# Kernel tuning notes

Hardware: AMD Instinct MI355X
Metric: run time of the kernel (lower is better)

Reference implementation:

```python
import jax, jax.numpy as jnp
import numpy as np

NEG_INF = float('-inf')

def setup_inputs() -> dict:
    key = jax.random.key(0)
    k1, k2 = jax.random.split(key)
    B, T, S, H, D = 2, 2048, 2048, 8, 64
    q = jax.random.normal(k1, (B, T, H, D), dtype=jnp.float32)
    kv = jax.random.normal(k2, (B, S, 2, H, D), dtype=jnp.float32)
    key_padding_mask = jnp.ones((B, S), dtype=bool)  # True = valid key
    return {"q": q, "kv": kv, "key_padding_mask": key_padding_mask, "causal": 1}


def reference(q, kv, key_padding_mask, causal):
    # q: (B,T,H,D), kv: (B,S,2,H,D)
    k = kv[:, :, 0]  # (B,S,H,D)
    v = kv[:, :, 1]  # (B,S,H,D)
    D = q.shape[-1]
    scale = D ** (-0.5)
    # scores: (B,H,T,S)
    scores = jnp.einsum('bthd,bshd->bhts', q, k) * scale
    # mask: True means "mask out" (matches torch masked_fill semantics)
    mask = ~key_padding_mask[:, None, None, :]  # (B,1,1,S)
    if causal:
        T, S = scores.shape[2], scores.shape[3]
        causal_mask = jnp.triu(jnp.ones((T, S), dtype=bool), k=1)  # (T,S)
        mask = mask | causal_mask[None, None, :, :]
    scores = jnp.where(mask, NEG_INF, scores)
    attn = jax.nn.softmax(scores, axis=-1)
    out = jnp.einsum('bhts,bshd->bthd', attn, v)  # (B,T,H,D)
    return out
```

## Files before the change

### kernel.cpp

```cpp
#include <hip/hip_runtime.h>
#include <hip/hip_bf16.h>

typedef __bf16 bf8_t __attribute__((ext_vector_type(8)));
typedef float  f4_t  __attribute__((ext_vector_type(4)));
typedef int    i4_t  __attribute__((ext_vector_type(4)));

constexpr int Bc = 2;
constexpr int Tc = 2048;
constexpr int Sc = 2048;
constexpr int Hc = 8;
constexpr int Dc = 64;
constexpr int BQ = 64;
constexpr int BK = 32;
constexpr int nQB = Tc / BQ;
constexpr int NKT = Sc / BK;
constexpr int NP  = nQB / 2;
constexpr int NS  = 4;
constexpr int TILE_H = 4096;
constexpr int KH = 2048;
constexpr int KTH = 4096;

__device__ __forceinline__ void g2l16(const void* g, void* l) {
    __builtin_amdgcn_global_load_lds(
        (const __attribute__((address_space(1))) void*)g,
        (__attribute__((address_space(3))) void*)l, 16, 0, 0);
}

__device__ __forceinline__ int pack_bf16(float lo, float hi) {
    const unsigned l16 = (unsigned)__builtin_bit_cast(unsigned short, (__bf16)lo);
    const unsigned h16 = (unsigned)__builtin_bit_cast(unsigned short, (__bf16)hi);
    return (int)(l16 | (h16 << 16));
}

__global__ __launch_bounds__(256)
void fa_prep(const float* __restrict__ kv, const int* __restrict__ kpm,
             __bf16* __restrict__ kvb, unsigned* __restrict__ kpmw)
{
    const int idx    = blockIdx.x * 256 + threadIdx.x;
    const int tile   = idx >> 9;
    const int within = idx & 511;
    const int b  = tile >> 9;
    const int h  = (tile >> 6) & 7;
    const int s0 = (tile & 63) * BK;
    __bf16* dst = kvb + (size_t)tile * TILE_H + within * 8;
    bf8_t o;
    if (within < 256) {
        const int row = within >> 3;
        const int col = ((within & 7) * 8) ^ ((row & 7) << 3);
        const float* src = kv + (((size_t)(b * Sc + s0 + row) * 2 + 0) * Hc + h) * Dc + col;
        const float4 x0 = *(const float4*)src;
        const float4 x1 = *(const float4*)(src + 4);
        o[0] = (__bf16)x0.x; o[1] = (__bf16)x0.y; o[2] = (__bf16)x0.z; o[3] = (__bf16)x0.w;
        o[4] = (__bf16)x1.x; o[5] = (__bf16)x1.y; o[6] = (__bf16)x1.z; o[7] = (__bf16)x1.w;
    } else {
        const int c    = within - 256;
        const int vrow = c >> 2;
        const int sc   = (c & 3) * 8;
        const float* src = kv + (((size_t)(b * Sc + s0 + sc) * 2 + 1) * Hc + h) * Dc + vrow;
        #pragma unroll
        for (int j = 0; j < 8; ++j) o[j] = (__bf16)src[(size_t)j * 2 * Hc * Dc];
    }
    *(bf8_t*)dst = o;

    if (idx < Bc * NKT) {
        const int bb = idx >> 6, tt = idx & 63;
        unsigned m = 0;
        for (int k = 0; k < 32; ++k)
            m |= (kpm[bb * Sc + tt * BK + k] != 0 ? 1u : 0u) << k;
        kpmw[idx] = m;
    }
}

__global__ __launch_bounds__(256, 4)
void fa_part(const float* __restrict__ q,
             const __bf16* __restrict__ kvb,
             const unsigned* __restrict__ kpmw,
             const int* __restrict__ causal_p,
             float* __restrict__ part_o,
             float* __restrict__ part_l)
{
    __shared__ __bf16 shK[3 * KTH];

    const int tid  = threadIdx.x;
    const int wave = tid >> 6;
    const int lane = tid & 63;
    const int n16  = lane & 15;
    const int quad = lane >> 4;

    const int bid = blockIdx.x;
    const int h   = bid & 7;
    const int g   = bid >> 3;
    const int b   = g / (NP * NS);
    const int rem = g % (NP * NS);
    const int p   = rem / NS;
    const int s   = rem % NS;
    const int causal = causal_p[0];

    const int nA   = causal ? (nQB - p)  : 32;
    const int nB   = causal ? (p + 1)    : 32;
    const int ntot = nA + nB;
    const int lo   = (ntot * s + NS - 1) / NS;
    const int hi   = (ntot * (s + 1) + NS - 1) / NS;

    const __bf16* kvt = kvb + (size_t)((b * Hc + h) * NKT) * TILE_H;
    const unsigned* mw_b = kpmw + b * NKT;

    const int kA_off = n16 * 64 + ((quad * 8) ^ ((n16 & 7) << 3));
    const int lds_st = tid * 8;
    const int vOff   = n16 * 32 + quad * 8;
    const int addrA  = (n16 + ((quad & 1) << 5)) << 2;
    const int addrB  = addrA + 64;
    const bool hiQ   = quad >= 2;
    const float scale = 0.125f;

    #pragma unroll 1
    for (int seg = 0; seg < 2; ++seg) {
        const int qt = seg ? p : (nQB - 1 - p);
        const int t0 = seg ? (max(lo, nA) - nA) : lo;
        const int t1 = seg ? (hi - nA)          : min(hi, nA);
        if (t0 >= t1) continue;

        __syncthreads();

        const int q_base = qt * BQ;
        const int tqn    = q_base + wave * 16 + n16;

        bf8_t a_q[2];
        {
            const float* qrow = q + ((size_t)(b * Tc + tqn) * Hc + h) * Dc;
            #pragma unroll
            for (int f = 0; f < 2; ++f) {
                const float4 x0 = *(const float4*)(qrow + f * 32 + quad * 8);
                const float4 x1 = *(const float4*)(qrow + f * 32 + quad * 8 + 4);
                bf8_t v;
                v[0] = (__bf16)(x0.x * scale); v[1] = (__bf16)(x0.y * scale);
                v[2] = (__bf16)(x0.z * scale); v[3] = (__bf16)(x0.w * scale);
                v[4] = (__bf16)(x1.x * scale); v[5] = (__bf16)(x1.y * scale);
                v[6] = (__bf16)(x1.z * scale); v[7] = (__bf16)(x1.w * scale);
                a_q[f] = v;
            }
        }

        f4_t o_acc[4];
        #pragma unroll
        for (int dt = 0; dt < 4; ++dt) o_acc[dt] = (f4_t){0.f, 0.f, 0.f, 0.f};
        float lsum = 0.f;

        int cu = 0, nx = KTH, nn = 2 * KTH;
        {
            const __bf16* src = kvt + (size_t)(2 * t0) * TILE_H;
            g2l16(src + lds_st,          &shK[lds_st]);
            g2l16(src + TILE_H + lds_st, &shK[2048 + lds_st]);
        }

        for (int it = t0; it < t1; ++it) {
            const int kb = it * 64;
            const unsigned cm0 = mw_b[2 * it];
            const unsigned cm1 = mw_b[2 * it + 1];

            const __bf16* vb0 = kvt + (size_t)(2 * it) * TILE_H + KH + vOff;
            const __bf16* vb1 = vb0 + TILE_H;
            const bf8_t bv0 = *(const bf8_t*)(vb0);
            const bf8_t bv1 = *(const bf8_t*)(vb0 + 512);
            const bf8_t bv2 = *(const bf8_t*)(vb0 + 1024);
            const bf8_t bv3 = *(const bf8_t*)(vb0 + 1536);

            if (it + 1 < t1) {
                const __bf16* srcn = kvt + (size_t)(2 * (it + 1)) * TILE_H;
                g2l16(srcn + lds_st,          &shK[nx + lds_st]);
                g2l16(srcn + TILE_H + lds_st, &shK[nx + 2048 + lds_st]);
                asm volatile("s_waitcnt vmcnt(6)" ::: "memory");
            } else {
                asm volatile("s_waitcnt vmcnt(4)" ::: "memory");
            }
            __builtin_amdgcn_s_barrier();

            const bf8_t bv4 = *(const bf8_t*)(vb1);
            const bf8_t bv5 = *(const bf8_t*)(vb1 + 512);
            const bf8_t bv6 = *(const bf8_t*)(vb1 + 1024);
            const bf8_t bv7 = *(const bf8_t*)(vb1 + 1536);

            #pragma unroll
            for (int hh = 0; hh < 2; ++hh) {
                const unsigned cmw = hh ? cm1 : cm0;
                int pk[2][2];
                #pragma unroll
                for (int sub = 0; sub < 2; ++sub) {
                    const int kbase = cu + hh * 2048 + sub * 1024;
                    const bf8_t bk0 = *(const bf8_t*)&shK[kbase + kA_off];
                    const bf8_t bk1 = *(const bf8_t*)&shK[kbase + (kA_off ^ 32)];
                    f4_t acc = (f4_t){0.f, 0.f, 0.f, 0.f};
                    __builtin_amdgcn_s_setprio(1);
                    acc = __builtin_amdgcn_mfma_f32_16x16x32_bf16(bk0, a_q[0], acc, 0, 0, 0);
                    acc = __builtin_amdgcn_mfma_f32_16x16x32_bf16(bk1, a_q[1], acc, 0, 0, 0);
                    __builtin_amdgcn_s_setprio(0);
                    const int keyb = kb + hh * 32 + sub * 16 + quad * 4;
                    const unsigned mb = cmw >> (sub * 16 + quad * 4);
                    float pv[4];
                    #pragma unroll
                    for (int r = 0; r < 4; ++r) {
                        const bool valid = ((mb >> r) & 1u) && (!causal || keyb + r <= tqn);
                        const float pp = valid ? __expf(acc[r] - 8.0f) : 0.0f;
                        lsum += pp;
                        pv[r] = pp;
                    }
                    pk[sub][0] = pack_bf16(pv[0], pv[1]);
                    pk[sub][1] = pack_bf16(pv[2], pv[3]);
                }

                const int a0 = __builtin_amdgcn_ds_bpermute(addrA, pk[0][0]);
                const int a1 = __builtin_amdgcn_ds_bpermute(addrA, pk[0][1]);
                const int b0 = __builtin_amdgcn_ds_bpermute(addrB, pk[0][0]);
                const int b1 = __builtin_amdgcn_ds_bpermute(addrB, pk[0][1]);
                const int c0 = __builtin_amdgcn_ds_bpermute(addrA, pk[1][0]);
                const int c1 = __builtin_amdgcn_ds_bpermute(addrA, pk[1][1]);
                const int d0 = __builtin_amdgcn_ds_bpermute(addrB, pk[1][0]);
                const int d1 = __builtin_amdgcn_ds_bpermute(addrB, pk[1][1]);
                union { i4_t i; bf8_t b; } u;
                u.i[0] = hiQ ? c0 : a0;
                u.i[1] = hiQ ? c1 : a1;
                u.i[2] = hiQ ? d0 : b0;
                u.i[3] = hiQ ? d1 : b1;
                const bf8_t a_p = u.b;

                __builtin_amdgcn_s_setprio(1);
                if (hh == 0) {
                    o_acc[0] = __builtin_amdgcn_mfma_f32_16x16x32_bf16(a_p, bv0, o_acc[0], 0, 0, 0);
                    o_acc[1] = __builtin_amdgcn_mfma_f32_16x16x32_bf16(a_p, bv1, o_acc[1], 0, 0, 0);
                    o_acc[2] = __builtin_amdgcn_mfma_f32_16x16x32_bf16(a_p, bv2, o_acc[2], 0, 0, 0);
                    o_acc[3] = __builtin_amdgcn_mfma_f32_16x16x32_bf16(a_p, bv3, o_acc[3], 0, 0, 0);
                } else {
                    o_acc[0] = __builtin_amdgcn_mfma_f32_16x16x32_bf16(a_p, bv4, o_acc[0], 0, 0, 0);
                    o_acc[1] = __builtin_amdgcn_mfma_f32_16x16x32_bf16(a_p, bv5, o_acc[1], 0, 0, 0);
                    o_acc[2] = __builtin_amdgcn_mfma_f32_16x16x32_bf16(a_p, bv6, o_acc[2], 0, 0, 0);
                    o_acc[3] = __builtin_amdgcn_mfma_f32_16x16x32_bf16(a_p, bv7, o_acc[3], 0, 0, 0);
                }
                __builtin_amdgcn_s_setprio(0);
            }

            const int tswap = cu; cu = nx; nx = nn; nn = tswap;
        }

        lsum += __shfl_xor(lsum, 16);
        lsum += __shfl_xor(lsum, 32);
        float l_row[4];
        #pragma unroll
        for (int r = 0; r < 4; ++r) {
            const int li = __builtin_amdgcn_ds_bpermute((quad * 4 + r) << 2,
                                                        __builtin_bit_cast(int, lsum));
            l_row[r] = __builtin_bit_cast(float, li);
        }

        const size_t slot = (size_t)(((b * Hc + h) * NP + p) * NS + s) * 2 + seg;
        float* po = part_o + slot * (BQ * Dc);
        #pragma unroll
        for (int dt = 0; dt < 4; ++dt) {
            #pragma unroll
            for (int r = 0; r < 4; ++r) {
                const int row = wave * 16 + quad * 4 + r;
                po[row * Dc + dt * 16 + n16] = o_acc[dt][r];
            }
        }
        if (n16 == 0) {
            #pragma unroll
            for (int r = 0; r < 4; ++r) {
                const int row = wave * 16 + quad * 4 + r;
                part_l[slot * BQ + row] = l_row[r];
            }
        }
    }
}

__global__ __launch_bounds__(256, 4)
void fa_reduce(const float* __restrict__ part_o,
               const float* __restrict__ part_l,
               const int* __restrict__ causal_p,
               float* __restrict__ out)
{
    const int gtid = blockIdx.x * 256 + threadIdx.x;
    const int e    = gtid & (BQ * Dc / 4 - 1);
    const int qi   = gtid >> 10;
    const int row  = e >> 4;
    const int d4   = e & 15;

    const int qt = qi & (nQB - 1);
    const int h  = (qi >> 5) & (Hc - 1);
    const int b  = qi >> 8;
    const int causal = causal_p[0];

    const int p    = (qt < NP) ? qt : (nQB - 1 - qt);
    const int seg  = (qt < NP) ? 1 : 0;
    const int nA   = causal ? (nQB - p) : 32;
    const int nB   = causal ? (p + 1)   : 32;
    const int ntot = nA + nB;
    const int segLo = seg ? nA : 0;
    const int segHi = seg ? ntot : nA;

    float4 acc = make_float4(0.f, 0.f, 0.f, 0.f);
    float  l   = 0.f;
    #pragma unroll
    for (int s = 0; s < NS; ++s) {
        const int lo = (ntot * s + NS - 1) / NS;
        const int hi = (ntot * (s + 1) + NS - 1) / NS;
        if (lo < segHi && segLo < hi && lo < hi) {
            const size_t slot = (size_t)(((b * Hc + h) * NP + p) * NS + s) * 2 + seg;
            const float4 v = *(const float4*)(part_o + slot * (BQ * Dc) + row * Dc + d4 * 4);
            acc.x += v.x; acc.y += v.y; acc.z += v.z; acc.w += v.w;
            l += part_l[slot * BQ + row];
        }
    }
    const float inv = 1.0f / l;
    const int t = qt * BQ + row;
    float4 o;
    o.x = acc.x * inv; o.y = acc.y * inv; o.z = acc.z * inv; o.w = acc.w * inv;
    *(float4*)(out + ((size_t)(b * Tc + t) * Hc + h) * Dc + d4 * 4) = o;
}

extern "C" void kernel_launch(void* const* d_in, const int* in_sizes, int n_in,
                              void* d_out, int out_size, void* d_ws, size_t ws_size,
                              hipStream_t stream) {
    const float* q   = (const float*)d_in[0];
    const float* kv  = (const float*)d_in[1];
    const int*   kpm = (const int*)d_in[2];
    const int*   cz  = (const int*)d_in[3];
    float*       out = (float*)d_out;

    __bf16* kvb = (__bf16*)d_ws;
    const size_t kvb_bytes = (size_t)Bc * Hc * NKT * TILE_H * sizeof(__bf16);
    unsigned* kpmw = (unsigned*)((char*)d_ws + kvb_bytes);
    float* part_o  = (float*)((char*)d_ws + kvb_bytes + 4096);

    const size_t nslots = (size_t)Bc * Hc * NP * NS * 2;
    float* part_l = part_o + nslots * (BQ * Dc);

    const int grid0 = Bc * Hc * NKT * 512 / 256;
    fa_prep<<<grid0, 256, 0, stream>>>(kv, kpm, kvb, kpmw);

    const int grid1 = Bc * Hc * NP * NS;
    fa_part<<<grid1, 256, 0, stream>>>(q, kvb, kpmw, cz, part_o, part_l);

    const int grid2 = (int)((size_t)Bc * Hc * nQB * (BQ * Dc / 4) / 256);
    fa_reduce<<<grid2, 256, 0, stream>>>(part_o, part_l, cz, out);
}
```

Measured before the change: 114.1 us.

## Stage V tiles through LDS with swizzled layout and double buffering

V tiles were previously loaded straight from global memory into registers each iteration. Now they are staged into LDS alongside K using async global-to-LDS copies, with the prep kernel writing V in a swizzled layout to avoid bank conflicts. The triple-buffered K ring becomes a double-buffered K+V slot, which adds a second barrier per iteration. The aim is to take the global-load latency for V off the critical path, at the cost of more LDS traffic and extra synchronisation.

```diff
diff --git a/kernel.cpp b/kernel.cpp
--- a/kernel.cpp
+++ b/kernel.cpp
@@ -18,7 +18,7 @@
 constexpr int NS  = 4;
 constexpr int TILE_H = 4096;
 constexpr int KH = 2048;
-constexpr int KTH = 4096;
+constexpr int SLOT_H = 8192;
 
 __device__ __forceinline__ void g2l16(const void* g, void* l) {
     __builtin_amdgcn_global_load_lds(
@@ -42,8 +42,8 @@
     const int b  = tile >> 9;
     const int h  = (tile >> 6) & 7;
     const int s0 = (tile & 63) * BK;
-    __bf16* dst = kvb + (size_t)tile * TILE_H + within * 8;
     bf8_t o;
+    __bf16* dst;
     if (within < 256) {
         const int row = within >> 3;
         const int col = ((within & 7) * 8) ^ ((row & 7) << 3);
@@ -52,13 +52,17 @@
         const float4 x1 = *(const float4*)(src + 4);
         o[0] = (__bf16)x0.x; o[1] = (__bf16)x0.y; o[2] = (__bf16)x0.z; o[3] = (__bf16)x0.w;
         o[4] = (__bf16)x1.x; o[5] = (__bf16)x1.y; o[6] = (__bf16)x1.z; o[7] = (__bf16)x1.w;
+        dst = kvb + (size_t)tile * TILE_H + within * 8;
     } else {
         const int c    = within - 256;
         const int vrow = c >> 2;
-        const int sc   = (c & 3) * 8;
-        const float* src = kv + (((size_t)(b * Sc + s0 + sc) * 2 + 1) * Hc + h) * Dc + vrow;
+        const int g8   = c & 3;
+        const float* src = kv + (((size_t)(b * Sc + s0 + g8 * 8) * 2 + 1) * Hc + h) * Dc + vrow;
         #pragma unroll
         for (int j = 0; j < 8; ++j) o[j] = (__bf16)src[(size_t)j * 2 * Hc * Dc];
+        const int r  = vrow >> 1;
+        const int gg = ((vrow & 1) * 4 + g8) ^ (r & 7);
+        dst = kvb + (size_t)tile * TILE_H + KH + r * 64 + gg * 8;
     }
     *(bf8_t*)dst = o;
 
@@ -79,7 +83,7 @@
              float* __restrict__ part_o,
              float* __restrict__ part_l)
 {
-    __shared__ __bf16 shK[3 * KTH];
+    __shared__ __bf16 shKV[2 * SLOT_H];
 
     const int tid  = threadIdx.x;
     const int wave = tid >> 6;
@@ -106,8 +110,9 @@
     const unsigned* mw_b = kpmw + b * NKT;
 
     const int kA_off = n16 * 64 + ((quad * 8) ^ ((n16 & 7) << 3));
+    const int vRd    = (n16 >> 1) * 64 +
+                       ((((n16 & 1) << 2) | quad) ^ (n16 >> 1)) * 8;
     const int lds_st = tid * 8;
-    const int vOff   = n16 * 32 + quad * 8;
     const int addrA  = (n16 + ((quad & 1) << 5)) << 2;
     const int addrB  = addrA + 64;
     const bool hiQ   = quad >= 2;
@@ -146,39 +151,32 @@
         for (int dt = 0; dt < 4; ++dt) o_acc[dt] = (f4_t){0.f, 0.f, 0.f, 0.f};
         float lsum = 0.f;
 
-        int cu = 0, nx = KTH, nn = 2 * KTH;
+        int cu = 0;
         {
             const __bf16* src = kvt + (size_t)(2 * t0) * TILE_H;
-            g2l16(src + lds_st,          &shK[lds_st]);
-            g2l16(src + TILE_H + lds_st, &shK[2048 + lds_st]);
+            g2l16(src + lds_st,               &shKV[lds_st]);
+            g2l16(src + TILE_H + lds_st,      &shKV[2048 + lds_st]);
+            g2l16(src + KH + lds_st,          &shKV[4096 + lds_st]);
+            g2l16(src + TILE_H + KH + lds_st, &shKV[6144 + lds_st]);
         }
 
         for (int it = t0; it < t1; ++it) {
             const int kb = it * 64;
             const unsigned cm0 = mw_b[2 * it];
             const unsigned cm1 = mw_b[2 * it + 1];
-
-            const __bf16* vb0 = kvt + (size_t)(2 * it) * TILE_H + KH + vOff;
-            const __bf16* vb1 = vb0 + TILE_H;
-            const bf8_t bv0 = *(const bf8_t*)(vb0);
-            const bf8_t bv1 = *(const bf8_t*)(vb0 + 512);
-            const bf8_t bv2 = *(const bf8_t*)(vb0 + 1024);
-            const bf8_t bv3 = *(const bf8_t*)(vb0 + 1536);
+            const int nx = cu ^ SLOT_H;
 
             if (it + 1 < t1) {
                 const __bf16* srcn = kvt + (size_t)(2 * (it + 1)) * TILE_H;
-                g2l16(srcn + lds_st,          &shK[nx + lds_st]);
-                g2l16(srcn + TILE_H + lds_st, &shK[nx + 2048 + lds_st]);
-                asm volatile("s_waitcnt vmcnt(6)" ::: "memory");
+                g2l16(srcn + lds_st,               &shKV[nx + lds_st]);
+                g2l16(srcn + TILE_H + lds_st,      &shKV[nx + 2048 + lds_st]);
+                g2l16(srcn + KH + lds_st,          &shKV[nx + 4096 + lds_st]);
+                g2l16(srcn + TILE_H + KH + lds_st, &shKV[nx + 6144 + lds_st]);
+                asm volatile("s_waitcnt vmcnt(4)" ::: "memory");
             } else {
-                asm volatile("s_waitcnt vmcnt(4)" ::: "memory");
+                asm volatile("s_waitcnt vmcnt(0)" ::: "memory");
             }
             __builtin_amdgcn_s_barrier();
-
-            const bf8_t bv4 = *(const bf8_t*)(vb1);
-            const bf8_t bv5 = *(const bf8_t*)(vb1 + 512);
-            const bf8_t bv6 = *(const bf8_t*)(vb1 + 1024);
-            const bf8_t bv7 = *(const bf8_t*)(vb1 + 1536);
 
             #pragma unroll
             for (int hh = 0; hh < 2; ++hh) {
@@ -187,8 +185,8 @@
                 #pragma unroll
                 for (int sub = 0; sub < 2; ++sub) {
                     const int kbase = cu + hh * 2048 + sub * 1024;
-                    const bf8_t bk0 = *(const bf8_t*)&shK[kbase + kA_off];
-                    const bf8_t bk1 = *(const bf8_t*)&shK[kbase + (kA_off ^ 32)];
+                    const bf8_t bk0 = *(const bf8_t*)&shKV[kbase + kA_off];
+                    const bf8_t bk1 = *(const bf8_t*)&shKV[kbase + (kA_off ^ 32)];
                     f4_t acc = (f4_t){0.f, 0.f, 0.f, 0.f};
                     __builtin_amdgcn_s_setprio(1);
                     acc = __builtin_amdgcn_mfma_f32_16x16x32_bf16(bk0, a_q[0], acc, 0, 0, 0);
@@ -223,22 +221,21 @@
                 u.i[3] = hiQ ? d1 : b1;
                 const bf8_t a_p = u.b;
 
+                const int vb = cu + 4096 + hh * 2048 + vRd;
+                const bf8_t bv0 = *(const bf8_t*)&shKV[vb];
+                const bf8_t bv1 = *(const bf8_t*)&shKV[vb + 512];
+                const bf8_t bv2 = *(const bf8_t*)&shKV[vb + 1024];
+                const bf8_t bv3 = *(const bf8_t*)&shKV[vb + 1536];
                 __builtin_amdgcn_s_setprio(1);
-                if (hh == 0) {
-                    o_acc[0] = __builtin_amdgcn_mfma_f32_16x16x32_bf16(a_p, bv0, o_acc[0], 0, 0, 0);
-                    o_acc[1] = __builtin_amdgcn_mfma_f32_16x16x32_bf16(a_p, bv1, o_acc[1], 0, 0, 0);
-                    o_acc[2] = __builtin_amdgcn_mfma_f32_16x16x32_bf16(a_p, bv2, o_acc[2], 0, 0, 0);
-                    o_acc[3] = __builtin_amdgcn_mfma_f32_16x16x32_bf16(a_p, bv3, o_acc[3], 0, 0, 0);
-                } else {
-                    o_acc[0] = __builtin_amdgcn_mfma_f32_16x16x32_bf16(a_p, bv4, o_acc[0], 0, 0, 0);
-                    o_acc[1] = __builtin_amdgcn_mfma_f32_16x16x32_bf16(a_p, bv5, o_acc[1], 0, 0, 0);
-                    o_acc[2] = __builtin_amdgcn_mfma_f32_16x16x32_bf16(a_p, bv6, o_acc[2], 0, 0, 0);
-                    o_acc[3] = __builtin_amdgcn_mfma_f32_16x16x32_bf16(a_p, bv7, o_acc[3], 0, 0, 0);
-                }
+                o_acc[0] = __builtin_amdgcn_mfma_f32_16x16x32_bf16(a_p, bv0, o_acc[0], 0, 0, 0);
+                o_acc[1] = __builtin_amdgcn_mfma_f32_16x16x32_bf16(a_p, bv1, o_acc[1], 0, 0, 0);
+                o_acc[2] = __builtin_amdgcn_mfma_f32_16x16x32_bf16(a_p, bv2, o_acc[2], 0, 0, 0);
+                o_acc[3] = __builtin_amdgcn_mfma_f32_16x16x32_bf16(a_p, bv3, o_acc[3], 0, 0, 0);
                 __builtin_amdgcn_s_setprio(0);
             }
 
-            const int tswap = cu; cu = nx; nx = nn; nn = tswap;
+            __builtin_amdgcn_s_barrier();
+            cu = nx;
         }
 
         lsum += __shfl_xor(lsum, 16);
```

After: 112.0 us. About the same (-1.9%).
